# Kernel optimization log

Measured on AMD Instinct MI355X. Metric: run time of the kernel, lower is better.

The kernel has to match this reference:

```python
import jax, jax.numpy as jnp
import numpy as np

T_DAYS = 1024   # forecast horizon (r_t length)
N_SAMP = 50000  # posterior_samples
J_WIN = 32      # transition_window


def setup_inputs() -> dict:
    key = jax.random.key(0)
    k0, k1, k2, k3, k4, k5 = jax.random.split(key, 6)
    # reproduction number around 1 so the recursion is numerically stable
    r_t = jax.random.uniform(k0, (T_DAYS,), minval=0.9, maxval=1.1, dtype=jnp.float32)
    # J days of warmup asymptomatic counts (one per posterior sample)
    warmup_A = jax.random.uniform(k1, (J_WIN, N_SAMP), minval=10.0, maxval=100.0, dtype=jnp.float32)
    # per-sample epidemiological parameters (reparameterized posterior samples)
    delta = jax.random.uniform(k2, (N_SAMP,), minval=0.95, maxval=1.0, dtype=jnp.float32)
    T_serial = jax.random.uniform(k3, (N_SAMP,), minval=4.0, maxval=7.0, dtype=jnp.float32)
    rho_M = jax.random.uniform(k4, (N_SAMP,), minval=0.05, maxval=0.3, dtype=jnp.float32)
    # lag distribution pi_M[j, s]: normalized over the J lags per sample
    pi_M = jax.nn.softmax(jax.random.normal(k5, (J_WIN, N_SAMP), dtype=jnp.float32), axis=0)
    return {"r_t": r_t, "warmup_A": warmup_A, "delta": delta,
            "T_serial": T_serial, "rho_M": rho_M, "pi_M": pi_M}


def reference(r_t, warmup_A, delta, T_serial, rho_M, pi_M):
    """Covid compartment forecast.

    A[day] = A[day-1] * delta * r_t[day]**(1/T_serial)   (sequential recursion)
    M[day] = sum_j A[day-1-j] * rho_M * pi_M[j]          (lagged transition window)
    Returns M: [T, S] incident mild cases per posterior sample.
    """
    J, S = warmup_A.shape
    T = r_t.shape[0]
    # per-day multiplicative growth factor, [T, S]
    growth = (r_t[:, None] ** (1.0 / T_serial)[None, :]) * delta[None, :]

    def step(a_prev, g):
        a = a_prev * g
        return a, a

    _, A_fc = jax.lax.scan(step, warmup_A[-1], growth)  # [T, S]
    A_full = jnp.concatenate([warmup_A, A_fc], axis=0)  # [J+T, S]

    # M[day] = sum_j A_full[J + day - 1 - j] * rho_M * pi_M[j]
    M = jnp.zeros((T, S), dtype=A_fc.dtype)
    for j in range(J):  # small fixed window, accumulate without [T,J,S] blowup
        start = J - 1 - j
        M = M + A_full[start:start + T] * (rho_M * pi_M[j])[None, :]
    return M
```

## Files before the change

### kernel.cpp

```cpp
#include <hip/hip_runtime.h>
#include <math.h>


#define T_DAYS 1024
#define J_WIN  32
#define DT     128
#define GROUPS (DT / 32)

typedef float f32x2 __attribute__((ext_vector_type(2)));

__global__ void prefix_log_kernel(const float* __restrict__ r_t,
                                  float* __restrict__ L) {
    __shared__ float buf[T_DAYS];
    const int i = threadIdx.x;
    buf[i] = __log2f(r_t[i]);
    __syncthreads();
    for (int off = 1; off < T_DAYS; off <<= 1) {
        float add = (i >= off) ? buf[i - off] : 0.0f;
        __syncthreads();
        buf[i] += add;
        __syncthreads();
    }
    L[i] = buf[i];
}

__device__ __forceinline__ float uload(const float* p) {
    return __uint_as_float(__builtin_amdgcn_readfirstlane(__float_as_uint(*p)));
}

__global__ __launch_bounds__(256, 2)
void covid_kernel(const float* __restrict__ warmup_A,
                  const float* __restrict__ delta_p,
                  const float* __restrict__ T_serial,
                  const float* __restrict__ rho_p,
                  const float* __restrict__ pi_M,
                  const float* __restrict__ L,
                  float* __restrict__ out,
                  int S) {
    const int p = blockIdx.x * 256 + threadIdx.x;
    const int s = 2 * p;
    if (s >= S) return;
    const int t0 = blockIdx.y * DT;

    const f32x2 Ts  = *(const f32x2*)&T_serial[s];
    const f32x2 dlt = *(const f32x2*)&delta_p[s];
    const f32x2 rho = *(const f32x2*)&rho_p[s];
    const f32x2 A0  = *(const f32x2*)&warmup_A[(J_WIN - 1) * S + s];
    f32x2 invT, ld;
    invT.x = 1.0f / Ts.x;        invT.y = 1.0f / Ts.y;
    ld.x   = __log2f(dlt.x);     ld.y   = __log2f(dlt.y);

    f32x2 rA0;
    rA0.x = rho.x * A0.x;  rA0.y = rho.y * A0.y;
    f32x2 w[J_WIN];
#pragma unroll
    for (int j = 0; j < J_WIN; ++j) {
        const f32x2 pi2 = *(const f32x2*)&pi_M[j * S + s];
        w[j].x = rA0.x * pi2.x;
        w[j].y = rA0.y * pi2.y;
    }

    f32x2 ring[J_WIN];
    if (t0 == 0) {
        f32x2 iA0;
        iA0.x = 1.0f / A0.x;  iA0.y = 1.0f / A0.y;
#pragma unroll
        for (int k = 0; k < J_WIN; ++k) {
            const f32x2 wa = *(const f32x2*)&warmup_A[k * S + s];
            ring[k].x = wa.x * iA0.x;
            ring[k].y = wa.y * iA0.y;
        }
    } else {
#pragma unroll
        for (int k = 0; k < J_WIN; ++k) {
            const float Lk = uload(&L[t0 - J_WIN + k]);
            const float dn = (float)(t0 - J_WIN + k + 1);
            ring[k].x = __builtin_amdgcn_exp2f(fmaf(invT.x, Lk, dn * ld.x));
            ring[k].y = __builtin_amdgcn_exp2f(fmaf(invT.y, Lk, dn * ld.y));
        }
    }

    f32x2 c;
    c.x = (float)(t0 + 1) * ld.x;
    c.y = (float)(t0 + 1) * ld.y;
    float* op = out + (size_t)t0 * S + s;
    int tg = t0;
#pragma unroll 1
    for (int g = 0; g < GROUPS; ++g) {
        float Lg[32];
#pragma unroll
        for (int k = 0; k < 32; ++k) Lg[k] = uload(&L[tg + k]);
#pragma unroll
        for (int u = 0; u < 32; ++u) {
            f32x2 m0 = {0.0f, 0.0f}, m1 = {0.0f, 0.0f};
            f32x2 m2 = {0.0f, 0.0f}, m3 = {0.0f, 0.0f};
#pragma unroll
            for (int j = 0; j < J_WIN; j += 4) {
                m0 = __builtin_elementwise_fma(w[j + 0], ring[(u - 1 - j) & 31], m0);
                m1 = __builtin_elementwise_fma(w[j + 1], ring[(u - 2 - j) & 31], m1);
                m2 = __builtin_elementwise_fma(w[j + 2], ring[(u - 3 - j) & 31], m2);
                m3 = __builtin_elementwise_fma(w[j + 3], ring[(u - 4 - j) & 31], m3);
            }
            f32x2 m;
            m.x = (m0.x + m1.x) + (m2.x + m3.x);
            m.y = (m0.y + m1.y) + (m2.y + m3.y);
            *(f32x2*)op = m;
            op += S;
            ring[u].x = __builtin_amdgcn_exp2f(fmaf(invT.x, Lg[u], c.x));
            ring[u].y = __builtin_amdgcn_exp2f(fmaf(invT.y, Lg[u], c.y));
            c.x += ld.x;
            c.y += ld.y;
        }
        tg += 32;
    }
}

extern "C" void kernel_launch(void* const* d_in, const int* in_sizes, int n_in,
                              void* d_out, int out_size, void* d_ws, size_t ws_size,
                              hipStream_t stream) {
    const float* r_t      = (const float*)d_in[0];
    const float* warmup_A = (const float*)d_in[1];
    const float* delta    = (const float*)d_in[2];
    const float* T_serial = (const float*)d_in[3];
    const float* rho_M    = (const float*)d_in[4];
    const float* pi_M     = (const float*)d_in[5];
    float* out = (float*)d_out;
    float* L   = (float*)d_ws;
    const int S = in_sizes[2];

    prefix_log_kernel<<<1, T_DAYS, 0, stream>>>(r_t, L);

    const int pairs = (S + 1) / 2;
    dim3 grid((pairs + 255) / 256, T_DAYS / DT);
    covid_kernel<<<grid, 256, 0, stream>>>(warmup_A, delta, T_serial, rho_M,
                                           pi_M, L, out, S);
}
```

Before: 241.3 us.

## Fuse prefix-log scan into main kernel and shrink block and time tiles

Removes the separate single-block prefix-sum launch. Each block now recomputes the log2 prefix sum of r_t into shared memory using a chunked per-thread scan plus a block scan. The block size drops to 128 threads and the time tile to 64 days, which doubles the grid in both dimensions. This removes one kernel launch and its serial dependency. In exchange, every block repeats the scan, each time tile carries relatively more warmup-ring recomputation, and the early-return before the scan's syncthreads is now placed after it.

Measured after the change: 240.6 us. About the same (-0.3%).

```diff
diff --git a/kernel.cpp b/kernel.cpp
--- a/kernel.cpp
+++ b/kernel.cpp
@@ -4,40 +4,53 @@
 
 #define T_DAYS 1024
 #define J_WIN  32
-#define DT     128
+#define DT     64
 #define GROUPS (DT / 32)
+#define BLK    128
+#define CHUNK  (T_DAYS / BLK)
 
 typedef float f32x2 __attribute__((ext_vector_type(2)));
 
-__global__ void prefix_log_kernel(const float* __restrict__ r_t,
-                                  float* __restrict__ L) {
-    __shared__ float buf[T_DAYS];
-    const int i = threadIdx.x;
-    buf[i] = __log2f(r_t[i]);
-    __syncthreads();
-    for (int off = 1; off < T_DAYS; off <<= 1) {
-        float add = (i >= off) ? buf[i - off] : 0.0f;
-        __syncthreads();
-        buf[i] += add;
-        __syncthreads();
-    }
-    L[i] = buf[i];
+__device__ __forceinline__ float sgpr_of(float x) {
+    return __uint_as_float(__builtin_amdgcn_readfirstlane(__float_as_uint(x)));
 }
 
-__device__ __forceinline__ float uload(const float* p) {
-    return __uint_as_float(__builtin_amdgcn_readfirstlane(__float_as_uint(*p)));
-}
-
-__global__ __launch_bounds__(256, 2)
-void covid_kernel(const float* __restrict__ warmup_A,
+__global__ __launch_bounds__(BLK, 2)
+void covid_kernel(const float* __restrict__ r_t,
+                  const float* __restrict__ warmup_A,
                   const float* __restrict__ delta_p,
                   const float* __restrict__ T_serial,
                   const float* __restrict__ rho_p,
                   const float* __restrict__ pi_M,
-                  const float* __restrict__ L,
                   float* __restrict__ out,
                   int S) {
-    const int p = blockIdx.x * 256 + threadIdx.x;
+    __shared__ float Lsh[T_DAYS];
+    __shared__ float tot[BLK];
+    const int tid = threadIdx.x;
+
+    float v[CHUNK];
+    {
+        const float* rp = r_t + tid * CHUNK;
+        float run = 0.0f;
+#pragma unroll
+        for (int k = 0; k < CHUNK; ++k) { run += __log2f(rp[k]); v[k] = run; }
+        tot[tid] = run;
+    }
+    __syncthreads();
+    for (int off = 1; off < BLK; off <<= 1) {
+        float add = (tid >= off) ? tot[tid - off] : 0.0f;
+        __syncthreads();
+        tot[tid] += add;
+        __syncthreads();
+    }
+    {
+        const float base = (tid > 0) ? tot[tid - 1] : 0.0f;
+#pragma unroll
+        for (int k = 0; k < CHUNK; ++k) Lsh[tid * CHUNK + k] = base + v[k];
+    }
+    __syncthreads();
+
+    const int p = blockIdx.x * BLK + tid;
     const int s = 2 * p;
     if (s >= S) return;
     const int t0 = blockIdx.y * DT;
@@ -73,7 +86,7 @@
     } else {
 #pragma unroll
         for (int k = 0; k < J_WIN; ++k) {
-            const float Lk = uload(&L[t0 - J_WIN + k]);
+            const float Lk = sgpr_of(Lsh[t0 - J_WIN + k]);
             const float dn = (float)(t0 - J_WIN + k + 1);
             ring[k].x = __builtin_amdgcn_exp2f(fmaf(invT.x, Lk, dn * ld.x));
             ring[k].y = __builtin_amdgcn_exp2f(fmaf(invT.y, Lk, dn * ld.y));
@@ -89,7 +102,7 @@
     for (int g = 0; g < GROUPS; ++g) {
         float Lg[32];
 #pragma unroll
-        for (int k = 0; k < 32; ++k) Lg[k] = uload(&L[tg + k]);
+        for (int k = 0; k < 32; ++k) Lg[k] = sgpr_of(Lsh[tg + k]);
 #pragma unroll
         for (int u = 0; u < 32; ++u) {
             f32x2 m0 = {0.0f, 0.0f}, m1 = {0.0f, 0.0f};
@@ -125,13 +138,10 @@
     const float* rho_M    = (const float*)d_in[4];
     const float* pi_M     = (const float*)d_in[5];
     float* out = (float*)d_out;
-    float* L   = (float*)d_ws;
     const int S = in_sizes[2];
 
-    prefix_log_kernel<<<1, T_DAYS, 0, stream>>>(r_t, L);
-
     const int pairs = (S + 1) / 2;
-    dim3 grid((pairs + 255) / 256, T_DAYS / DT);
-    covid_kernel<<<grid, 256, 0, stream>>>(warmup_A, delta, T_serial, rho_M,
-                                           pi_M, L, out, S);
+    dim3 grid((pairs + BLK - 1) / BLK, T_DAYS / DT);
+    covid_kernel<<<grid, BLK, 0, stream>>>(r_t, warmup_A, delta, T_serial,
+                                           rho_M, pi_M, out, S);
 }
```
